# Kernel optimization log

Hardware: AMD Instinct MI355X
Metric: run time of the kernel (lower is better)

## Reference

```python
import jax, jax.numpy as jnp
import numpy as np
from jax import lax

B, H_ENC, E, H, V, T = 64, 512, 512, 1024, 32000, 64
SOS, EOS = 1, 2


def setup_inputs() -> dict:
    key = jax.random.key(0)
    ks = jax.random.split(key, 7)
    s = 0.05
    return {
        "encoder_hidden": jax.random.normal(ks[0], (2, B, H_ENC), jnp.float32),
        "embedding": jax.random.normal(ks[1], (V, E), jnp.float32) * s,
        "Wh_w": jax.random.normal(ks[2], (H, 2 * H_ENC), jnp.float32) * s,
        "Wh_b": jnp.zeros((H,), jnp.float32),
        "W_ih": jax.random.normal(ks[3], (3 * H, E + 2 * H_ENC), jnp.float32) * s,
        "W_hh": jax.random.normal(ks[4], (3 * H, H), jnp.float32) * s,
        "b_ih": jnp.zeros((3 * H,), jnp.float32),
        "b_hh": jnp.zeros((3 * H,), jnp.float32),
        "out_w": jax.random.normal(ks[5], (V, H), jnp.float32) * s,
        "out_b": jnp.zeros((V,), jnp.float32),
    }


def reference(encoder_hidden, embedding, Wh_w, Wh_b, W_ih, W_hh, b_ih, b_hh, out_w, out_b):
    # initialize_forward: [2,B,H_enc] -> transpose -> [B,2,H_enc] -> reshape [1,B,2*H_enc] -> Wh
    flat = encoder_hidden.transpose(1, 0, 2).reshape(B, 2 * H_ENC)  # [B, 1024]
    h0 = flat @ Wh_w.T + Wh_b  # [B, H]
    # _get_context: hidden[-2:] permuted -> [B,2,H_enc] -> reshape [B, 2*H_enc] (constant per step)
    context = flat  # same flattening, num_layers of encoder hidden == 2 (bidirectional)

    def gru_cell(x, h):
        # PyTorch GRU cell: gates order (r, z, n)
        gi = x @ W_ih.T + b_ih  # [B, 3H]
        gh = h @ W_hh.T + b_hh  # [B, 3H]
        i_r, i_z, i_n = jnp.split(gi, 3, axis=-1)
        h_r, h_z, h_n = jnp.split(gh, 3, axis=-1)
        r = jax.nn.sigmoid(i_r + h_r)
        z = jax.nn.sigmoid(i_z + h_z)
        n = jnp.tanh(i_n + r * h_n)
        return (1.0 - z) * n + z * h

    def step(carry, _):
        inp, h, finished = carry  # inp [B] int32, h [B,H], finished [B] bool
        x = embedding[inp]  # [B, E]
        gru_in = jnp.concatenate([x, context], axis=-1)  # [B, E + 2*H_enc]
        h = gru_cell(gru_in, h)
        logits = h @ out_w.T + out_b  # [B, V]  (dropout p=0 -> identity)
        tok = jnp.argmax(logits, axis=-1).astype(jnp.int32)  # topk k=1 greedy
        finished = finished | (tok == EOS)
        inp_next = jnp.where(finished, EOS, tok)  # masked_fill with eos
        return (inp_next, h, finished), tok

    init = (jnp.full((B,), SOS, jnp.int32), h0, jnp.zeros((B,), bool))
    (inp, h_final, fin), toks = lax.scan(step, init, None, length=T)  # toks [T, B]
    decoder_outputs = toks.T  # [B, T]  (torch.stack(outputs).T)
    decoder_hidden = h_final[None]  # [1, B, H]
    return decoder_outputs, decoder_hidden
```

## Files before the change

kernel.cpp:

```cpp
#include <hip/hip_runtime.h>
#include <math.h>

#define BB   64
#define HENC 512
#define EE   512
#define HH   1024
#define VV   32000
#define TT   64
#define G3   3072
#define SOS_TOK 1
#define EOS_TOK 2
#define KSEG 128
#define NP2  4000
#define GHB  192

typedef __attribute__((ext_vector_type(8))) short short8;
typedef __attribute__((ext_vector_type(8))) unsigned short ushort8;
typedef __attribute__((ext_vector_type(4))) float f32x4;
typedef unsigned short ushort;
typedef unsigned int uint;

#define OFF_FLATT 0u
#define OFF_XT    65536u
#define OFF_HT    98304u
#define OFF_GC    163840u
#define OFF_P     360448u
#define OFF_PH    1933312u
#define OFF_PMAX  2457600u
#define OFF_PIDX  2713600u
#define OFF_FIN   2969600u
#define OFF_HA    2969728u
#define OFF_WB    3002496u
#define OFF_END   19386496u
#define NEED_BYTES ((size_t)OFF_END * 4u)

__device__ __forceinline__ ushort f2bf(float x) {
  uint u = __float_as_uint(x);
  u = u + 0x7fffu + ((u >> 16) & 1u);
  return (ushort)(u >> 16);
}

__global__ __launch_bounds__(256) void k_setup(const float* __restrict__ enc,
                                               const float* __restrict__ emb,
                                               float* __restrict__ flatT,
                                               float* __restrict__ xT,
                                               int* __restrict__ fin0) {
  int idx = blockIdx.x * 256 + threadIdx.x;
  int j = idx >> 6, b = idx & 63;
  float v = (j < 512) ? enc[b * 512 + j] : enc[32768 + b * 512 + (j - 512)];
  flatT[j * 64 + b] = v;
  if (j < 512) xT[j * 64 + b] = emb[SOS_TOK * EE + j];
  if (idx < 64) fin0[idx] = 0;
}

__global__ __launch_bounds__(256) void k_packWb(const float* __restrict__ W,
                                                ushort* __restrict__ Wb) {
  int t = blockIdx.x * 256 + threadIdx.x;
  int l = t & 63, kc = (t >> 6) & 31, nt = t >> 11;
  int n = nt * 16 + (l & 15);
  int k = kc * 32 + ((l >> 4) << 3);
  const float* src = W + (size_t)n * 1024 + k;
  ushort8 r;
  #pragma unroll
  for (int j = 0; j < 8; ++j) r[j] = f2bf(src[j]);
  *(ushort8*)(Wb + (size_t)t * 8) = r;
}

__global__ __launch_bounds__(256) void k_gemm(const float* __restrict__ AT,
                                              const float* __restrict__ W,
                                              int ldw, int wofs,
                                              float* __restrict__ C, int N) {
  __shared__ float Ws[KSEG][65];
  int tid = threadIdx.x;
  int n0 = blockIdx.x * 64;
  int k0 = blockIdx.y * KSEG;

  #pragma unroll
  for (int r = 0; r < 8; ++r) {
    int f4 = tid + 256 * r;
    int n = f4 >> 5, kq = f4 & 31;
    float4 w4 = *(const float4*)&W[(size_t)(n0 + n) * ldw + wofs + k0 + 4 * kq];
    Ws[4 * kq + 0][n] = w4.x;
    Ws[4 * kq + 1][n] = w4.y;
    Ws[4 * kq + 2][n] = w4.z;
    Ws[4 * kq + 3][n] = w4.w;
  }
  __syncthreads();

  int wv = __builtin_amdgcn_readfirstlane(tid >> 6);
  int lane = tid & 63;
  int mb = wv * 16;

  float acc[16];
  #pragma unroll
  for (int i = 0; i < 16; ++i) acc[i] = 0.f;

  #pragma unroll 4
  for (int kk = 0; kk < KSEG; ++kk) {
    float w = Ws[kk][lane];
    const float* a = &AT[(size_t)(k0 + kk) * 64 + mb];
    float av[16];
    *(float4*)&av[0]  = *(const float4*)(a + 0);
    *(float4*)&av[4]  = *(const float4*)(a + 4);
    *(float4*)&av[8]  = *(const float4*)(a + 8);
    *(float4*)&av[12] = *(const float4*)(a + 12);
    #pragma unroll
    for (int i = 0; i < 16; ++i) acc[i] += av[i] * w;
  }

  float* dst = C + ((size_t)blockIdx.y * 64 + mb) * N + n0 + lane;
  #pragma unroll
  for (int i = 0; i < 16; ++i) dst[(size_t)i * N] = acc[i];
}

__global__ __launch_bounds__(256) void k_gates(const float* __restrict__ xT,
                                               const float* __restrict__ hT,
                                               const float* __restrict__ Wih,
                                               const float* __restrict__ Whh,
                                               float* __restrict__ P,
                                               int base_by) {
  __shared__ float Ws[KSEG][65];
  int tid = threadIdx.x;
  int n0 = blockIdx.x * 64;
  int by = blockIdx.y + base_by;
  bool gi = (by < 4);
  const float* AT = gi ? xT : hT;
  const float* W  = gi ? Wih : Whh;
  int ldw = gi ? 1536 : 1024;
  int nsegs = gi ? 1 : 2;
  int k0base = gi ? by * KSEG : (by - 4) * 256;

  int wv = __builtin_amdgcn_readfirstlane(tid >> 6);
  int lane = tid & 63;
  int mb = wv * 16;

  float acc[16];
  #pragma unroll
  for (int i = 0; i < 16; ++i) acc[i] = 0.f;

  for (int s = 0; s < nsegs; ++s) {
    int k0 = k0base + s * KSEG;
    if (s) __syncthreads();
    #pragma unroll
    for (int r = 0; r < 8; ++r) {
      int f4 = tid + 256 * r;
      int n = f4 >> 5, kq = f4 & 31;
      float4 w4 = *(const float4*)&W[(size_t)(n0 + n) * ldw + k0 + 4 * kq];
      Ws[4 * kq + 0][n] = w4.x;
      Ws[4 * kq + 1][n] = w4.y;
      Ws[4 * kq + 2][n] = w4.z;
      Ws[4 * kq + 3][n] = w4.w;
    }
    __syncthreads();
    #pragma unroll 4
    for (int kk = 0; kk < KSEG; ++kk) {
      float w = Ws[kk][lane];
      const float* a = &AT[(size_t)(k0 + kk) * 64 + mb];
      float av[16];
      *(float4*)&av[0]  = *(const float4*)(a + 0);
      *(float4*)&av[4]  = *(const float4*)(a + 4);
      *(float4*)&av[8]  = *(const float4*)(a + 8);
      *(float4*)&av[12] = *(const float4*)(a + 12);
      #pragma unroll
      for (int i = 0; i < 16; ++i) acc[i] += av[i] * w;
    }
  }

  float* dst = P + ((size_t)by * 64 + mb) * G3 + n0 + lane;
  #pragma unroll
  for (int i = 0; i < 16; ++i) dst[(size_t)i * G3] = acc[i];
}

__global__ __launch_bounds__(256) void k_reduce_gc(const float* __restrict__ P,
                                                   const float* __restrict__ b_ih,
                                                   float* __restrict__ gc) {
  int idx = blockIdx.x * 256 + threadIdx.x;
  int n = idx % G3;
  float s = b_ih[n];
  #pragma unroll
  for (int p = 0; p < 8; ++p) s += P[(size_t)p * (64 * G3) + idx];
  gc[idx] = s;
}

__device__ __forceinline__ void packH1(float v, int b, int g, ushort* hA) {
  int kc = g >> 5, q = (g >> 3) & 3, j = g & 7;
  int lane = (q << 4) | (b & 15), mt = b >> 4;
  size_t fi = ((size_t)((mt * 32 + kc) * 64 + lane)) * 8 + j;
  hA[fi] = f2bf(v);
}

__global__ __launch_bounds__(256) void k_reduce_h0(const float* __restrict__ Ph,
                                                   const float* __restrict__ Wh_b,
                                                   float* __restrict__ hT,
                                                   ushort* __restrict__ hA) {
  int idx = blockIdx.x * 256 + threadIdx.x;
  int b = idx >> 10, g = idx & 1023;
  float s = Wh_b[g];
  #pragma unroll
  for (int p = 0; p < 8; ++p) s += Ph[(size_t)p * 65536 + idx];
  hT[g * 64 + b] = s;
  packH1(s, b, g, hA);
}

__global__ __launch_bounds__(256) void k_combine(const float* __restrict__ P,
                                                 const float* __restrict__ gc,
                                                 const float* __restrict__ b_hh,
                                                 float* __restrict__ hT,
                                                 ushort* __restrict__ hA) {
  int b = blockIdx.x >> 2;
  int g = ((blockIdx.x & 3) << 8) + threadIdx.x;
  float ir = gc[b * G3 + g];
  float iz = gc[b * G3 + 1024 + g];
  float in_ = gc[b * G3 + 2048 + g];
  float hr = b_hh[g], hz = b_hh[1024 + g], hn = b_hh[2048 + g];
  #pragma unroll
  for (int p = 0; p < 4; ++p) {
    const float* row = P + ((size_t)p * 64 + b) * G3;
    ir += row[g]; iz += row[1024 + g]; in_ += row[2048 + g];
  }
  #pragma unroll
  for (int p = 4; p < 8; ++p) {
    const float* row = P + ((size_t)p * 64 + b) * G3;
    hr += row[g]; hz += row[1024 + g]; hn += row[2048 + g];
  }
  float rr = 1.f / (1.f + expf(-(ir + hr)));
  float zz = 1.f / (1.f + expf(-(iz + hz)));
  float nn = tanhf(in_ + rr * hn);
  float hold = hT[g * 64 + b];
  float hnew = (1.f - zz) * nn + zz * hold;
  hT[g * 64 + b] = hnew;
  packH1(hnew, b, g, hA);
}

__device__ __forceinline__ short8 cvt8(const float* p) {
  float4 x = *(const float4*)p;
  float4 y = *(const float4*)(p + 4);
  short8 r;
  r[0] = (short)f2bf(x.x); r[1] = (short)f2bf(x.y);
  r[2] = (short)f2bf(x.z); r[3] = (short)f2bf(x.w);
  r[4] = (short)f2bf(y.x); r[5] = (short)f2bf(y.y);
  r[6] = (short)f2bf(y.z); r[7] = (short)f2bf(y.w);
  return r;
}

template <bool PACKED>
__global__ __launch_bounds__(256) void k_logits(const ushort* __restrict__ Wb,
                                                const float* __restrict__ Wf,
                                                const ushort* __restrict__ hA,
                                                const float* __restrict__ bo,
                                                float* __restrict__ pmax,
                                                int* __restrict__ pidx,
                                                const float* __restrict__ hT,
                                                const float* __restrict__ Whh,
                                                float* __restrict__ P) {
  __shared__ float Ws[KSEG][65];
  int tid = threadIdx.x, wv = tid >> 6, lane = tid & 63;

  if (blockIdx.x < GHB) {
    int bx = blockIdx.x;
    int by = bx / 48;
    int n0 = (bx % 48) * 64;
    int slot = 4 + by;
    int k0base = by * 256;

    int wvs = __builtin_amdgcn_readfirstlane(wv);
    int mb = wvs * 16;

    float acc[16];
    #pragma unroll
    for (int i = 0; i < 16; ++i) acc[i] = 0.f;

    for (int s = 0; s < 2; ++s) {
      int k0 = k0base + s * KSEG;
      if (s) __syncthreads();
      #pragma unroll
      for (int r = 0; r < 8; ++r) {
        int f4 = tid + 256 * r;
        int n = f4 >> 5, kq = f4 & 31;
        float4 w4 = *(const float4*)&Whh[(size_t)(n0 + n) * 1024 + k0 + 4 * kq];
        Ws[4 * kq + 0][n] = w4.x;
        Ws[4 * kq + 1][n] = w4.y;
        Ws[4 * kq + 2][n] = w4.z;
        Ws[4 * kq + 3][n] = w4.w;
      }
      __syncthreads();
      #pragma unroll 4
      for (int kk = 0; kk < KSEG; ++kk) {
        float w = Ws[kk][lane];
        const float* a = &hT[(size_t)(k0 + kk) * 64 + mb];
        float av[16];
        *(float4*)&av[0]  = *(const float4*)(a + 0);
        *(float4*)&av[4]  = *(const float4*)(a + 4);
        *(float4*)&av[8]  = *(const float4*)(a + 8);
        *(float4*)&av[12] = *(const float4*)(a + 12);
        #pragma unroll
        for (int i = 0; i < 16; ++i) acc[i] += av[i] * w;
      }
    }

    float* dst = P + ((size_t)slot * 64 + mb) * G3 + n0 + lane;
    #pragma unroll
    for (int i = 0; i < 16; ++i) dst[(size_t)i * G3] = acc[i];
    return;
  }

  int nt = (blockIdx.x - GHB) * 4 + wv;
  int nl = lane & 15, q = lane >> 4;

  const short8* Bp = (const short8*)Wb + ((size_t)nt * 2048 + lane);
  const float*  Bf = Wf + (size_t)(nt * 16 + nl) * 1024 + (q << 3);
  const short8* Ap = (const short8*)hA + lane;

  f32x4 acc[4];
  #pragma unroll
  for (int m = 0; m < 4; ++m) acc[m] = (f32x4){0.f, 0.f, 0.f, 0.f};

  short8 bR[4], aR[4][4];
  #pragma unroll
  for (int d = 0; d < 4; ++d) {
    bR[d] = PACKED ? Bp[d * 64] : cvt8(Bf + d * 32);
    #pragma unroll
    for (int m = 0; m < 4; ++m) aR[d][m] = Ap[(m * 32 + d) * 64];
  }

  #pragma unroll
  for (int kc = 0; kc < 32; ++kc) {
    const int sl = kc & 3;
    #pragma unroll
    for (int m = 0; m < 4; ++m)
      acc[m] = __builtin_amdgcn_mfma_f32_16x16x32_bf16(aR[sl][m], bR[sl], acc[m], 0, 0, 0);
    if (kc < 28) {
      bR[sl] = PACKED ? Bp[(kc + 4) * 64] : cvt8(Bf + (kc + 4) * 32);
      #pragma unroll
      for (int m = 0; m < 4; ++m) aR[sl][m] = Ap[(m * 32 + kc + 4) * 64];
    }
  }

  float bias = bo[nt * 16 + nl];
  int myn = nt * 16 + nl;
  #pragma unroll
  for (int mt = 0; mt < 4; ++mt) {
    #pragma unroll
    for (int r = 0; r < 4; ++r) {
      float v1 = acc[mt][r] + bias; int i1 = myn;
      float v2 = -3.402823466e38f;  int i2 = 0x7fffffff;
      #pragma unroll
      for (int s = 1; s < 16; s <<= 1) {
        float ov1 = __shfl_xor(v1, s, 64); int oi1 = __shfl_xor(i1, s, 64);
        float ov2 = __shfl_xor(v2, s, 64); int oi2 = __shfl_xor(i2, s, 64);
        bool take = (ov1 > v1) || (ov1 == v1 && oi1 < i1);
        float n1v = take ? ov1 : v1; int n1i = take ? oi1 : i1;
        float cav = take ? v1 : ov1; int cai = take ? i1 : oi1;
        float cbv = take ? ov2 : v2; int cbi = take ? oi2 : i2;
        bool bb = (cbv > cav) || (cbv == cav && cbi < cai);
        v1 = n1v; i1 = n1i;
        v2 = bb ? cbv : cav; i2 = bb ? cbi : cai;
      }
      if (nl == 0) {
        int m = mt * 16 + q * 4 + r;
        pmax[(size_t)m * NP2 + nt * 2 + 0] = v1;
        pidx[(size_t)m * NP2 + nt * 2 + 0] = i1;
        pmax[(size_t)m * NP2 + nt * 2 + 1] = v2;
        pidx[(size_t)m * NP2 + nt * 2 + 1] = i2;
      }
    }
  }
}

__global__ __launch_bounds__(256) void k_finish(const float* __restrict__ pmax,
                                                const int* __restrict__ pidx,
                                                const float* __restrict__ hT,
                                                const float* __restrict__ Wf,
                                                const float* __restrict__ bo,
                                                const float* __restrict__ emb,
                                                const int* __restrict__ fin_old,
                                                int* __restrict__ fin_new,
                                                float* __restrict__ xT,
                                                float* __restrict__ tok_out, int t) {
  __shared__ float bv[256];
  __shared__ int   bi[256];
  __shared__ int    sch[4];
  __shared__ double ssc[4];
  __shared__ int    sinp;
  int b = blockIdx.x, tid = threadIdx.x;

  float cv[16]; int ci[16];
  if (tid < 250) {
    const float* pm = pmax + (size_t)b * NP2 + tid * 16;
    const int*   pi = pidx + (size_t)b * NP2 + tid * 16;
    #pragma unroll
    for (int j4 = 0; j4 < 4; ++j4) {
      float4 v4 = *(const float4*)(pm + j4 * 4);
      int4   i4 = *(const int4*)(pi + j4 * 4);
      cv[j4 * 4 + 0] = v4.x; ci[j4 * 4 + 0] = i4.x;
      cv[j4 * 4 + 1] = v4.y; ci[j4 * 4 + 1] = i4.y;
      cv[j4 * 4 + 2] = v4.z; ci[j4 * 4 + 2] = i4.z;
      cv[j4 * 4 + 3] = v4.w; ci[j4 * 4 + 3] = i4.w;
    }
  } else {
    #pragma unroll
    for (int j = 0; j < 16; ++j) { cv[j] = -3.402823466e38f; ci[j] = 0x7fffffff; }
  }

  int ch0 = -1, ch1 = -1, ch2 = -1;
  for (int r = 0; r < 4; ++r) {
    float v = -3.402823466e38f; int id = 0x7fffffff;
    #pragma unroll
    for (int j = 0; j < 16; ++j) {
      bool ex = (ci[j] == ch0) | (ci[j] == ch1) | (ci[j] == ch2);
      if (!ex && (cv[j] > v || (cv[j] == v && ci[j] < id))) { v = cv[j]; id = ci[j]; }
    }
    bv[tid] = v; bi[tid] = id;
    __syncthreads();
    for (int s = 128; s > 0; s >>= 1) {
      if (tid < s) {
        float ov = bv[tid + s]; int oi = bi[tid + s];
        if (ov > bv[tid] || (ov == bv[tid] && oi < bi[tid])) { bv[tid] = ov; bi[tid] = oi; }
      }
      __syncthreads();
    }
    if (tid == 0) sch[r] = bi[0];
    __syncthreads();
    int c = sch[r];
    if (r == 0) ch0 = c; else if (r == 1) ch1 = c; else if (r == 2) ch2 = c;
  }

  int c = tid >> 6, ln = tid & 63;
  int cid = sch[c];
  double s = 0.0;
  #pragma unroll 4
  for (int k = ln; k < 1024; k += 64)
    s += (double)hT[k * 64 + b] * (double)Wf[(size_t)cid * 1024 + k];
  #pragma unroll
  for (int sh = 1; sh < 64; sh <<= 1) s += __shfl_xor(s, sh, 64);
  if (ln == 0) ssc[c] = s + (double)bo[cid];
  __syncthreads();

  if (tid == 0) {
    double bs = ssc[0]; int bid = sch[0];
    #pragma unroll
    for (int j = 1; j < 4; ++j)
      if (ssc[j] > bs || (ssc[j] == bs && sch[j] < bid)) { bs = ssc[j]; bid = sch[j]; }
    int tok = bid;
    int f = fin_old[b] | (tok == EOS_TOK ? 1 : 0);
    tok_out[b * TT + t] = (float)tok;
    fin_new[b] = f;
    sinp = f ? EOS_TOK : tok;
  }
  __syncthreads();
  int inp = sinp;
  xT[tid * 64 + b]         = emb[(size_t)inp * EE + tid];
  xT[(tid + 256) * 64 + b] = emb[(size_t)inp * EE + tid + 256];
}

__global__ __launch_bounds__(256) void k_hout(const float* __restrict__ hT,
                                              float* __restrict__ outH) {
  int idx = blockIdx.x * 256 + threadIdx.x;
  int b = idx >> 10, g = idx & 1023;
  outH[idx] = hT[g * 64 + b];
}

extern "C" void kernel_launch(void* const* d_in, const int* in_sizes, int n_in,
                              void* d_out, int out_size, void* d_ws, size_t ws_size,
                              hipStream_t stream) {
  const float* enc   = (const float*)d_in[0];
  const float* emb   = (const float*)d_in[1];
  const float* Wh_w  = (const float*)d_in[2];
  const float* Wh_b  = (const float*)d_in[3];
  const float* W_ih  = (const float*)d_in[4];
  const float* W_hh  = (const float*)d_in[5];
  const float* b_ih  = (const float*)d_in[6];
  const float* b_hh  = (const float*)d_in[7];
  const float* out_w = (const float*)d_in[8];
  const float* out_b = (const float*)d_in[9];

  float* ws    = (float*)d_ws;
  float* flatT = ws + OFF_FLATT;
  float* xT    = ws + OFF_XT;
  float* hT    = ws + OFF_HT;
  float* gc    = ws + OFF_GC;
  float* P     = ws + OFF_P;
  float* Ph    = ws + OFF_PH;
  float* pmax  = ws + OFF_PMAX;
  int*   pidx  = (int*)(ws + OFF_PIDX);
  int*   fin   = (int*)(ws + OFF_FIN);
  ushort* hA   = (ushort*)(ws + OFF_HA);
  ushort* Wb   = (ushort*)(ws + OFF_WB);

  float* outTok = (float*)d_out;
  float* outH   = (float*)d_out + BB * TT;

  const bool packed = (ws_size >= NEED_BYTES);

  k_setup<<<256, 256, 0, stream>>>(enc, emb, flatT, xT, fin);
  if (packed) k_packWb<<<16000, 256, 0, stream>>>(out_w, Wb);
  k_gemm<<<dim3(48, 8), 256, 0, stream>>>(flatT, W_ih, 1536, 512, P, G3);
  k_reduce_gc<<<768, 256, 0, stream>>>(P, b_ih, gc);
  k_gemm<<<dim3(16, 8), 256, 0, stream>>>(flatT, Wh_w, 1024, 0, Ph, HH);
  k_reduce_h0<<<256, 256, 0, stream>>>(Ph, Wh_b, hT, hA);
  k_gates<<<dim3(48, 4), 256, 0, stream>>>(xT, hT, W_ih, W_hh, P, 4);

  for (int t = 0; t < TT; ++t) {
    k_gates<<<dim3(48, 4), 256, 0, stream>>>(xT, hT, W_ih, W_hh, P, 0);
    k_combine<<<256, 256, 0, stream>>>(P, gc, b_hh, hT, hA);
    if (packed)
      k_logits<true><<<500 + GHB, 256, 0, stream>>>(Wb, out_w, hA, out_b, pmax, pidx,
                                                    hT, W_hh, P);
    else
      k_logits<false><<<500 + GHB, 256, 0, stream>>>(Wb, out_w, hA, out_b, pmax, pidx,
                                                     hT, W_hh, P);
    k_finish<<<64, 256, 0, stream>>>(pmax, pidx, hT, out_w, out_b, emb,
                                     fin + (t & 1) * 64, fin + ((t + 1) & 1) * 64,
                                     xT, outTok, t);
  }
  k_hout<<<256, 256, 0, stream>>>(hT, outH);
}
```

Before: 4.158 ms.

## Double per-wave logits tiles, register top-4 finish, row-major h copy

Each wave in the logits kernel now computes two 16-column vocab tiles, reusing the loaded hidden-state A fragments across both. This halves the logits block count and the redundant A loads. The finish kernel replaces four rounds of shared-memory tree reduction with a per-thread top-4 insertion, then a wave shuffle merge and a single-thread merge across waves. A row-major copy of h is kept so the double-precision rescoring and the final output read contiguous float4 data. The costs are higher register pressure in the logits kernel and fewer blocks to hide memory latency.

```diff
diff --git a/kernel.cpp b/kernel.cpp
--- a/kernel.cpp
+++ b/kernel.cpp
@@ -13,6 +13,7 @@
 #define KSEG 128
 #define NP2  4000
 #define GHB  192
+#define LOGB 250
 
 typedef __attribute__((ext_vector_type(8))) short short8;
 typedef __attribute__((ext_vector_type(8))) unsigned short ushort8;
@@ -30,15 +31,21 @@
 #define OFF_PIDX  2713600u
 #define OFF_FIN   2969600u
 #define OFF_HA    2969728u
-#define OFF_WB    3002496u
-#define OFF_END   19386496u
+#define OFF_HB    3002496u
+#define OFF_WB    3068032u
+#define OFF_END   19452032u
 #define NEED_BYTES ((size_t)OFF_END * 4u)
+
+#define NEG_INF (-3.402823466e38f)
+#define IDX_INF 0x7fffffff
 
 __device__ __forceinline__ ushort f2bf(float x) {
   uint u = __float_as_uint(x);
   u = u + 0x7fffu + ((u >> 16) & 1u);
   return (ushort)(u >> 16);
 }
+
+#define BETTER(av, ai, bv, bi) ((av) > (bv) || ((av) == (bv) && (ai) < (bi)))
 
 __global__ __launch_bounds__(256) void k_setup(const float* __restrict__ enc,
                                                const float* __restrict__ emb,
@@ -192,6 +199,7 @@
 __global__ __launch_bounds__(256) void k_reduce_h0(const float* __restrict__ Ph,
                                                    const float* __restrict__ Wh_b,
                                                    float* __restrict__ hT,
+                                                   float* __restrict__ hB,
                                                    ushort* __restrict__ hA) {
   int idx = blockIdx.x * 256 + threadIdx.x;
   int b = idx >> 10, g = idx & 1023;
@@ -199,6 +207,7 @@
   #pragma unroll
   for (int p = 0; p < 8; ++p) s += Ph[(size_t)p * 65536 + idx];
   hT[g * 64 + b] = s;
+  hB[idx] = s;
   packH1(s, b, g, hA);
 }
 
@@ -206,6 +215,7 @@
                                                  const float* __restrict__ gc,
                                                  const float* __restrict__ b_hh,
                                                  float* __restrict__ hT,
+                                                 float* __restrict__ hB,
                                                  ushort* __restrict__ hA) {
   int b = blockIdx.x >> 2;
   int g = ((blockIdx.x & 3) << 8) + threadIdx.x;
@@ -229,6 +239,7 @@
   float hold = hT[g * 64 + b];
   float hnew = (1.f - zz) * nn + zz * hold;
   hT[g * 64 + b] = hnew;
+  hB[b * 1024 + g] = hnew;
   packH1(hnew, b, g, hA);
 }
 
@@ -241,6 +252,41 @@
   r[4] = (short)f2bf(y.x); r[5] = (short)f2bf(y.y);
   r[6] = (short)f2bf(y.z); r[7] = (short)f2bf(y.w);
   return r;
+}
+
+__device__ __forceinline__ void top2_epilogue(const f32x4* acc, int nt, int nl, int q,
+                                              const float* __restrict__ bo,
+                                              float* __restrict__ pmax,
+                                              int* __restrict__ pidx) {
+  float bias = bo[nt * 16 + nl];
+  int myn = nt * 16 + nl;
+  #pragma unroll
+  for (int mt = 0; mt < 4; ++mt) {
+    #pragma unroll
+    for (int r = 0; r < 4; ++r) {
+      float v1 = acc[mt][r] + bias; int i1 = myn;
+      float v2 = NEG_INF;           int i2 = IDX_INF;
+      #pragma unroll
+      for (int s = 1; s < 16; s <<= 1) {
+        float ov1 = __shfl_xor(v1, s, 64); int oi1 = __shfl_xor(i1, s, 64);
+        float ov2 = __shfl_xor(v2, s, 64); int oi2 = __shfl_xor(i2, s, 64);
+        bool take = BETTER(ov1, oi1, v1, i1);
+        float n1v = take ? ov1 : v1; int n1i = take ? oi1 : i1;
+        float cav = take ? v1 : ov1; int cai = take ? i1 : oi1;
+        float cbv = take ? ov2 : v2; int cbi = take ? oi2 : i2;
+        bool bb = BETTER(cbv, cbi, cav, cai);
+        v1 = n1v; i1 = n1i;
+        v2 = bb ? cbv : cav; i2 = bb ? cbi : cai;
+      }
+      if (nl == 0) {
+        int m = mt * 16 + q * 4 + r;
+        pmax[(size_t)m * NP2 + nt * 2 + 0] = v1;
+        pidx[(size_t)m * NP2 + nt * 2 + 0] = i1;
+        pmax[(size_t)m * NP2 + nt * 2 + 1] = v2;
+        pidx[(size_t)m * NP2 + nt * 2 + 1] = i2;
+      }
+    }
+  }
 }
 
 template <bool PACKED>
@@ -304,21 +350,27 @@
     return;
   }
 
-  int nt = (blockIdx.x - GHB) * 4 + wv;
+  int nt0 = (((blockIdx.x - GHB) * 4 + wv) << 1);
   int nl = lane & 15, q = lane >> 4;
 
-  const short8* Bp = (const short8*)Wb + ((size_t)nt * 2048 + lane);
-  const float*  Bf = Wf + (size_t)(nt * 16 + nl) * 1024 + (q << 3);
+  const short8* Bp0 = (const short8*)Wb + ((size_t)nt0 * 2048 + lane);
+  const short8* Bp1 = Bp0 + 2048;
+  const float*  Bf0 = Wf + (size_t)(nt0 * 16 + nl) * 1024 + (q << 3);
+  const float*  Bf1 = Bf0 + 16 * 1024;
   const short8* Ap = (const short8*)hA + lane;
 
-  f32x4 acc[4];
-  #pragma unroll
-  for (int m = 0; m < 4; ++m) acc[m] = (f32x4){0.f, 0.f, 0.f, 0.f};
-
-  short8 bR[4], aR[4][4];
+  f32x4 acc0[4], acc1[4];
+  #pragma unroll
+  for (int m = 0; m < 4; ++m) {
+    acc0[m] = (f32x4){0.f, 0.f, 0.f, 0.f};
+    acc1[m] = (f32x4){0.f, 0.f, 0.f, 0.f};
+  }
+
+  short8 b0R[4], b1R[4], aR[4][4];
   #pragma unroll
   for (int d = 0; d < 4; ++d) {
-    bR[d] = PACKED ? Bp[d * 64] : cvt8(Bf + d * 32);
+    b0R[d] = PACKED ? Bp0[d * 64] : cvt8(Bf0 + d * 32);
+    b1R[d] = PACKED ? Bp1[d * 64] : cvt8(Bf1 + d * 32);
     #pragma unroll
     for (int m = 0; m < 4; ++m) aR[d][m] = Ap[(m * 32 + d) * 64];
   }
@@ -328,48 +380,25 @@
     const int sl = kc & 3;
     #pragma unroll
     for (int m = 0; m < 4; ++m)
-      acc[m] = __builtin_amdgcn_mfma_f32_16x16x32_bf16(aR[sl][m], bR[sl], acc[m], 0, 0, 0);
+      acc0[m] = __builtin_amdgcn_mfma_f32_16x16x32_bf16(aR[sl][m], b0R[sl], acc0[m], 0, 0, 0);
+    #pragma unroll
+    for (int m = 0; m < 4; ++m)
+      acc1[m] = __builtin_amdgcn_mfma_f32_16x16x32_bf16(aR[sl][m], b1R[sl], acc1[m], 0, 0, 0);
     if (kc < 28) {
-      bR[sl] = PACKED ? Bp[(kc + 4) * 64] : cvt8(Bf + (kc + 4) * 32);
+      b0R[sl] = PACKED ? Bp0[(kc + 4) * 64] : cvt8(Bf0 + (kc + 4) * 32);
+      b1R[sl] = PACKED ? Bp1[(kc + 4) * 64] : cvt8(Bf1 + (kc + 4) * 32);
       #pragma unroll
       for (int m = 0; m < 4; ++m) aR[sl][m] = Ap[(m * 32 + kc + 4) * 64];
     }
   }
 
-  float bias = bo[nt * 16 + nl];
-  int myn = nt * 16 + nl;
-  #pragma unroll
-  for (int mt = 0; mt < 4; ++mt) {
-    #pragma unroll
-    for (int r = 0; r < 4; ++r) {
-      float v1 = acc[mt][r] + bias; int i1 = myn;
-      float v2 = -3.402823466e38f;  int i2 = 0x7fffffff;
-      #pragma unroll
-      for (int s = 1; s < 16; s <<= 1) {
-        float ov1 = __shfl_xor(v1, s, 64); int oi1 = __shfl_xor(i1, s, 64);
-        float ov2 = __shfl_xor(v2, s, 64); int oi2 = __shfl_xor(i2, s, 64);
-        bool take = (ov1 > v1) || (ov1 == v1 && oi1 < i1);
-        float n1v = take ? ov1 : v1; int n1i = take ? oi1 : i1;
-        float cav = take ? v1 : ov1; int cai = take ? i1 : oi1;
-        float cbv = take ? ov2 : v2; int cbi = take ? oi2 : i2;
-        bool bb = (cbv > cav) || (cbv == cav && cbi < cai);
-        v1 = n1v; i1 = n1i;
-        v2 = bb ? cbv : cav; i2 = bb ? cbi : cai;
-      }
-      if (nl == 0) {
-        int m = mt * 16 + q * 4 + r;
-        pmax[(size_t)m * NP2 + nt * 2 + 0] = v1;
-        pidx[(size_t)m * NP2 + nt * 2 + 0] = i1;
-        pmax[(size_t)m * NP2 + nt * 2 + 1] = v2;
-        pidx[(size_t)m * NP2 + nt * 2 + 1] = i2;
-      }
-    }
-  }
+  top2_epilogue(acc0, nt0 + 0, nl, q, bo, pmax, pidx);
+  top2_epilogue(acc1, nt0 + 1, nl, q, bo, pmax, pidx);
 }
 
 __global__ __launch_bounds__(256) void k_finish(const float* __restrict__ pmax,
                                                 const int* __restrict__ pidx,
-                                                const float* __restrict__ hT,
+                                                const float* __restrict__ hB,
                                                 const float* __restrict__ Wf,
                                                 const float* __restrict__ bo,
                                                 const float* __restrict__ emb,
@@ -377,60 +406,105 @@
                                                 int* __restrict__ fin_new,
                                                 float* __restrict__ xT,
                                                 float* __restrict__ tok_out, int t) {
-  __shared__ float bv[256];
-  __shared__ int   bi[256];
+  __shared__ float  sv[16];
+  __shared__ int    si[16];
   __shared__ int    sch[4];
   __shared__ double ssc[4];
   __shared__ int    sinp;
   int b = blockIdx.x, tid = threadIdx.x;
-
-  float cv[16]; int ci[16];
+  int wv = tid >> 6, ln = tid & 63;
+
+  float v0 = NEG_INF, v1 = NEG_INF, v2 = NEG_INF, v3 = NEG_INF;
+  int   i0 = IDX_INF, i1 = IDX_INF, i2 = IDX_INF, i3 = IDX_INF;
+
+  #define INS4(cv, ci)                                                   \
+    {                                                                    \
+      bool c0 = BETTER(cv, ci, v0, i0);                                  \
+      bool c1 = BETTER(cv, ci, v1, i1);                                  \
+      bool c2 = BETTER(cv, ci, v2, i2);                                  \
+      bool c3 = BETTER(cv, ci, v3, i3);                                  \
+      v3 = c3 ? (c2 ? v2 : (cv)) : v3;  i3 = c3 ? (c2 ? i2 : (ci)) : i3; \
+      v2 = c2 ? (c1 ? v1 : (cv)) : v2;  i2 = c2 ? (c1 ? i1 : (ci)) : i2; \
+      v1 = c1 ? (c0 ? v0 : (cv)) : v1;  i1 = c1 ? (c0 ? i0 : (ci)) : i1; \
+      v0 = c0 ? (cv) : v0;              i0 = c0 ? (ci) : i0;             \
+    }
+
   if (tid < 250) {
     const float* pm = pmax + (size_t)b * NP2 + tid * 16;
     const int*   pi = pidx + (size_t)b * NP2 + tid * 16;
     #pragma unroll
     for (int j4 = 0; j4 < 4; ++j4) {
-      float4 v4 = *(const float4*)(pm + j4 * 4);
-      int4   i4 = *(const int4*)(pi + j4 * 4);
-      cv[j4 * 4 + 0] = v4.x; ci[j4 * 4 + 0] = i4.x;
-      cv[j4 * 4 + 1] = v4.y; ci[j4 * 4 + 1] = i4.y;
-      cv[j4 * 4 + 2] = v4.z; ci[j4 * 4 + 2] = i4.z;
-      cv[j4 * 4 + 3] = v4.w; ci[j4 * 4 + 3] = i4.w;
-    }
-  } else {
-    #pragma unroll
-    for (int j = 0; j < 16; ++j) { cv[j] = -3.402823466e38f; ci[j] = 0x7fffffff; }
-  }
-
-  int ch0 = -1, ch1 = -1, ch2 = -1;
-  for (int r = 0; r < 4; ++r) {
-    float v = -3.402823466e38f; int id = 0x7fffffff;
-    #pragma unroll
-    for (int j = 0; j < 16; ++j) {
-      bool ex = (ci[j] == ch0) | (ci[j] == ch1) | (ci[j] == ch2);
-      if (!ex && (cv[j] > v || (cv[j] == v && ci[j] < id))) { v = cv[j]; id = ci[j]; }
-    }
-    bv[tid] = v; bi[tid] = id;
-    __syncthreads();
-    for (int s = 128; s > 0; s >>= 1) {
-      if (tid < s) {
-        float ov = bv[tid + s]; int oi = bi[tid + s];
-        if (ov > bv[tid] || (ov == bv[tid] && oi < bi[tid])) { bv[tid] = ov; bi[tid] = oi; }
-      }
-      __syncthreads();
-    }
-    if (tid == 0) sch[r] = bi[0];
-    __syncthreads();
-    int c = sch[r];
-    if (r == 0) ch0 = c; else if (r == 1) ch1 = c; else if (r == 2) ch2 = c;
-  }
-
-  int c = tid >> 6, ln = tid & 63;
+      float4 c4 = *(const float4*)(pm + j4 * 4);
+      int4   x4 = *(const int4*)(pi + j4 * 4);
+      INS4(c4.x, x4.x);
+      INS4(c4.y, x4.y);
+      INS4(c4.z, x4.z);
+      INS4(c4.w, x4.w);
+    }
+  }
+
+  #define CESW(xv, xi, yv, yi)                                     \
+    {                                                              \
+      bool sw_ = BETTER(yv, yi, xv, xi);                           \
+      float tv_ = xv; int ti_ = xi;                                \
+      xv = sw_ ? yv : xv;  xi = sw_ ? yi : xi;                     \
+      yv = sw_ ? tv_ : yv; yi = sw_ ? ti_ : yi;                    \
+    }
+
+  for (int s = 1; s < 64; s <<= 1) {
+    float w0 = __shfl_xor(v0, s, 64), w1 = __shfl_xor(v1, s, 64);
+    float w2 = __shfl_xor(v2, s, 64), w3 = __shfl_xor(v3, s, 64);
+    int   j0 = __shfl_xor(i0, s, 64), j1 = __shfl_xor(i1, s, 64);
+    int   j2 = __shfl_xor(i2, s, 64), j3 = __shfl_xor(i3, s, 64);
+    if (BETTER(w3, j3, v0, i0)) { v0 = w3; i0 = j3; }
+    if (BETTER(w2, j2, v1, i1)) { v1 = w2; i1 = j2; }
+    if (BETTER(w1, j1, v2, i2)) { v2 = w1; i2 = j1; }
+    if (BETTER(w0, j0, v3, i3)) { v3 = w0; i3 = j0; }
+    CESW(v0, i0, v2, i2);
+    CESW(v1, i1, v3, i3);
+    CESW(v0, i0, v1, i1);
+    CESW(v2, i2, v3, i3);
+  }
+
+  if (ln == 0) {
+    sv[wv * 4 + 0] = v0; si[wv * 4 + 0] = i0;
+    sv[wv * 4 + 1] = v1; si[wv * 4 + 1] = i1;
+    sv[wv * 4 + 2] = v2; si[wv * 4 + 2] = i2;
+    sv[wv * 4 + 3] = v3; si[wv * 4 + 3] = i3;
+  }
+  __syncthreads();
+
+  if (tid == 0) {
+    float t0 = NEG_INF, t1 = NEG_INF, t2 = NEG_INF, t3 = NEG_INF;
+    int   x0 = IDX_INF, x1 = IDX_INF, x2 = IDX_INF, x3 = IDX_INF;
+    #pragma unroll
+    for (int e = 0; e < 16; ++e) {
+      float cv = sv[e]; int ci = si[e];
+      bool c0 = BETTER(cv, ci, t0, x0);
+      bool c1 = BETTER(cv, ci, t1, x1);
+      bool c2 = BETTER(cv, ci, t2, x2);
+      bool c3 = BETTER(cv, ci, t3, x3);
+      t3 = c3 ? (c2 ? t2 : cv) : t3;  x3 = c3 ? (c2 ? x2 : ci) : x3;
+      t2 = c2 ? (c1 ? t1 : cv) : t2;  x2 = c2 ? (c1 ? x1 : ci) : x2;
+      t1 = c1 ? (c0 ? t0 : cv) : t1;  x1 = c1 ? (c0 ? x0 : ci) : x1;
+      t0 = c0 ? cv : t0;              x0 = c0 ? ci : x0;
+    }
+    sch[0] = x0; sch[1] = x1; sch[2] = x2; sch[3] = x3;
+  }
+  __syncthreads();
+
+  int c = wv;
   int cid = sch[c];
+  const float4* hv4 = (const float4*)(hB + (size_t)b * 1024);
+  const float4* wv4 = (const float4*)(Wf + (size_t)cid * 1024);
   double s = 0.0;
-  #pragma unroll 4
-  for (int k = ln; k < 1024; k += 64)
-    s += (double)hT[k * 64 + b] * (double)Wf[(size_t)cid * 1024 + k];
+  #pragma unroll
+  for (int j = 0; j < 4; ++j) {
+    float4 hx = hv4[j * 64 + ln];
+    float4 wx = wv4[j * 64 + ln];
+    s += (double)hx.x * (double)wx.x + (double)hx.y * (double)wx.y +
+         (double)hx.z * (double)wx.z + (double)hx.w * (double)wx.w;
+  }
   #pragma unroll
   for (int sh = 1; sh < 64; sh <<= 1) s += __shfl_xor(s, sh, 64);
   if (ln == 0) ssc[c] = s + (double)bo[cid];
@@ -453,11 +527,10 @@
   xT[(tid + 256) * 64 + b] = emb[(size_t)inp * EE + tid + 256];
 }
 
-__global__ __launch_bounds__(256) void k_hout(const float* __restrict__ hT,
+__global__ __launch_bounds__(256) void k_hout(const float* __restrict__ hB,
                                               float* __restrict__ outH) {
   int idx = blockIdx.x * 256 + threadIdx.x;
-  int b = idx >> 10, g = idx & 1023;
-  outH[idx] = hT[g * 64 + b];
+  outH[idx] = hB[idx];
 }
 
 extern "C" void kernel_launch(void* const* d_in, const int* in_sizes, int n_in,
@@ -485,6 +558,7 @@
   int*   pidx  = (int*)(ws + OFF_PIDX);
   int*   fin   = (int*)(ws + OFF_FIN);
   ushort* hA   = (ushort*)(ws + OFF_HA);
+  float* hB    = ws + OFF_HB;
   ushort* Wb   = (ushort*)(ws + OFF_WB);
 
   float* outTok = (float*)d_out;
@@ -497,21 +571,21 @@
   k_gemm<<<dim3(48, 8), 256, 0, stream>>>(flatT, W_ih, 1536, 512, P, G3);
   k_reduce_gc<<<768, 256, 0, stream>>>(P, b_ih, gc);
   k_gemm<<<dim3(16, 8), 256, 0, stream>>>(flatT, Wh_w, 1024, 0, Ph, HH);
-  k_reduce_h0<<<256, 256, 0, stream>>>(Ph, Wh_b, hT, hA);
+  k_reduce_h0<<<256, 256, 0, stream>>>(Ph, Wh_b, hT, hB, hA);
   k_gates<<<dim3(48, 4), 256, 0, stream>>>(xT, hT, W_ih, W_hh, P, 4);
 
   for (int t = 0; t < TT; ++t) {
     k_gates<<<dim3(48, 4), 256, 0, stream>>>(xT, hT, W_ih, W_hh, P, 0);
-    k_combine<<<256, 256, 0, stream>>>(P, gc, b_hh, hT, hA);
+    k_combine<<<256, 256, 0, stream>>>(P, gc, b_hh, hT, hB, hA);
     if (packed)
-      k_logits<true><<<500 + GHB, 256, 0, stream>>>(Wb, out_w, hA, out_b, pmax, pidx,
-                                                    hT, W_hh, P);
+      k_logits<true><<<LOGB + GHB, 256, 0, stream>>>(Wb, out_w, hA, out_b, pmax, pidx,
+                                                     hT, W_hh, P);
     else
-      k_logits<false><<<500 + GHB, 256, 0, stream>>>(Wb, out_w, hA, out_b, pmax, pidx,
-                                                     hT, W_hh, P);
-    k_finish<<<64, 256, 0, stream>>>(pmax, pidx, hT, out_w, out_b, emb,
+      k_logits<false><<<LOGB + GHB, 256, 0, stream>>>(Wb, out_w, hA, out_b, pmax, pidx,
+                                                      hT, W_hh, P);
+    k_finish<<<64, 256, 0, stream>>>(pmax, pidx, hB, out_w, out_b, emb,
                                      fin + (t & 1) * 64, fin + ((t + 1) & 1) * 64,
                                      xT, outTok, t);
   }
-  k_hout<<<256, 256, 0, stream>>>(hT, outH);
-}
+  k_hout<<<256, 256, 0, stream>>>(hB, outH);
+}
```

After: 4.377 ms. +5.3%, slower.
